# Kernel tuning notes

Measured on AMD Instinct MI355X. Metric: run time of the kernel, lower is better.

Reference implementation:

```python
import jax, jax.numpy as jnp
import numpy as np

D_MODEL = 1024
NUM_HEADS = 16
D_K = D_MODEL // NUM_HEADS
B, S = 4, 2048


def setup_inputs() -> dict:
    key = jax.random.key(0)
    ks = jax.random.split(key, 12)
    scale = 1.0 / np.sqrt(D_MODEL)
    inp = {
        "query": jax.random.normal(ks[0], (B, S, D_MODEL), jnp.float32),
        "key": jax.random.normal(ks[1], (B, S, D_MODEL), jnp.float32),
        "value": jax.random.normal(ks[2], (B, S, D_MODEL), jnp.float32),
        # causal mask, broadcastable over (batch, heads)
        "mask": jnp.tril(jnp.ones((S, S), jnp.int32))[None, None, :, :],
        "Wq": jax.random.normal(ks[3], (D_MODEL, D_MODEL), jnp.float32) * scale,
        "bq": jnp.zeros((D_MODEL,), jnp.float32),
        "Wk": jax.random.normal(ks[4], (D_MODEL, D_MODEL), jnp.float32) * scale,
        "bk": jnp.zeros((D_MODEL,), jnp.float32),
        "Wv": jax.random.normal(ks[5], (D_MODEL, D_MODEL), jnp.float32) * scale,
        "bv": jnp.zeros((D_MODEL,), jnp.float32),
        "Wo": jax.random.normal(ks[6], (D_MODEL, D_MODEL), jnp.float32) * scale,
        "bo": jnp.zeros((D_MODEL,), jnp.float32),
    }
    return inp


def reference(query, key, value, mask, Wq, bq, Wk, bk, Wv, bv, Wo, bo):
    b = query.shape[0]
    # projections (torch Linear: x @ W.T + b)
    Q = query @ Wq.T + bq
    K = key @ Wk.T + bk
    V = value @ Wv.T + bv
    # [B, S, D] -> [B, H, S, d_k]
    def split_heads(x):
        return x.reshape(b, -1, NUM_HEADS, D_K).transpose(0, 2, 1, 3)
    Q, K, V = split_heads(Q), split_heads(K), split_heads(V)
    # scaled dot-product attention, full score matrix as in original
    scores = jnp.einsum("bhqd,bhkd->bhqk", Q, K) / jnp.sqrt(jnp.float32(D_K))
    scores = jnp.where(mask == 0, jnp.float32(-jnp.inf), scores)
    attn = jax.nn.softmax(scores, axis=-1)  # dropout p=0.0 -> identity
    x = jnp.einsum("bhqk,bhkd->bhqd", attn, V)
    # [B, H, S, d_k] -> [B, S, D]
    x = x.transpose(0, 2, 1, 3).reshape(b, -1, D_MODEL)
    return x @ Wo.T + bo
```

## Files before the change

### kernel.cpp

```cpp
#include <hip/hip_runtime.h>
#include <hip/hip_bf16.h>
#include <stdint.h>

#define D_MODEL 1024
#define NUM_HEADS 16
#define DK 64
#define BATCH 4
#define SEQ 2048
#define MTOT (BATCH * SEQ)

typedef unsigned short u16;
typedef unsigned int u32;
typedef __bf16 bf16x8 __attribute__((ext_vector_type(8)));
typedef float f32x4 __attribute__((ext_vector_type(4)));
typedef short s16x4 __attribute__((ext_vector_type(4)));
typedef int   i32x4 __attribute__((ext_vector_type(4)));
typedef int   i32x2 __attribute__((ext_vector_type(2)));
typedef uint  u32x2 __attribute__((ext_vector_type(2)));

__device__ __forceinline__ f32x4 mfma16(s16x4 a, s16x4 b, f32x4 c) {
  return __builtin_amdgcn_mfma_f32_16x16x16bf16_1k(a, b, c, 0, 0, 0);
}

__device__ __forceinline__ u16 f2bf(float f) {
  union { float f; unsigned u; } c; c.f = f;
  unsigned u = c.u + 0x7fffu + ((c.u >> 16) & 1u);
  return (u16)(u >> 16);
}
__device__ __forceinline__ u32 pack_bf2(float f0, float f1) {
  return __builtin_amdgcn_perm(__float_as_uint(f1), __float_as_uint(f0), 0x07060302u);
}
__device__ __forceinline__ s16x4 cast_s16x4(u32 lo, u32 hi) {
  u32x2 t = {lo, hi};
  return (s16x4)t;
}

__device__ __forceinline__ void async16(void* g, void* lds) {
  __builtin_amdgcn_global_load_lds(
      (__attribute__((address_space(1))) void*)g,
      (__attribute__((address_space(3))) void*)lds,
      16, 0, 0);
}
__device__ __forceinline__ void vm_drain() {
  asm volatile("s_waitcnt vmcnt(0)" ::: "memory");
}

struct CvtArgs {
  const float* s[7];
  u16* d[7];
  int n[7];
};
__global__ __launch_bounds__(256)
void cvt_multi(CvtArgs a) {
  const int which = blockIdx.y;
  const int n = a.n[which];
  const int i = (blockIdx.x * 256 + threadIdx.x) * 8;
  if (i >= n) return;
  const float* s = a.s[which];
  u16* d = a.d[which];
  const float4 x = *(const float4*)(s + i);
  const float4 y = *(const float4*)(s + i + 4);
  *(ushort4*)(d + i)     = make_ushort4(f2bf(x.x), f2bf(x.y), f2bf(x.z), f2bf(x.w));
  *(ushort4*)(d + i + 4) = make_ushort4(f2bf(y.x), f2bf(y.y), f2bf(y.z), f2bf(y.w));
}

struct GBatch {
  const u16* A[3]; const u16* W[3]; const float* bias[3];
  void* C[3]; float osc[3]; int mode[3];
};
__global__ __launch_bounds__(256, 2)
void gemm_bt_bias(GBatch ga)
{
  __shared__ __align__(16) u16 smem[16896];
  u16* As0 = smem;
  u16* Bs0 = smem + 4096;
  u16* As1 = smem + 8192;
  u16* Bs1 = smem + 12288;

  const int z = blockIdx.z;
  const u16* __restrict__ A = ga.A[z];
  const u16* __restrict__ W = ga.W[z];
  const float* __restrict__ bias = ga.bias[z];
  void* __restrict__ Cv = ga.C[z];
  const float oscale = ga.osc[z];
  const int mode = ga.mode[z];

  const int t = threadIdx.x;
  const int w = t >> 6, l = t & 63;
  const int quad = l >> 4, lane16 = l & 15;
  const int m0 = blockIdx.x * 128;
  const int n0 = blockIdx.y * 128;
  const int wm = (w >> 1) * 64, wn = (w & 1) * 64;

  const int srow = t >> 2;
  const int scol = (t & 3) * 8;
  const u16* Ag = A + (long)(m0 + srow) * D_MODEL + scol;
  const u16* Wg = W + (long)(n0 + srow) * D_MODEL + scol;

  f32x4 acc[4][4] = {};

  auto stage = [&](u16* As_, u16* Bs_, int k0) {
    async16((void*)(Ag + k0), As_ + w * 512);
    async16((void*)(Ag + 64 * D_MODEL + k0), As_ + w * 512 + 2048);
    async16((void*)(Wg + k0), Bs_ + w * 512);
    async16((void*)(Wg + 64 * D_MODEL + k0), Bs_ + w * 512 + 2048);
  };
  auto compute = [&](const u16* As_, const u16* Bs_) {
    bf16x8 af[4], bfr[4];
#pragma unroll
    for (int i = 0; i < 4; ++i)
      af[i] = *(const bf16x8*)&As_[(wm + i * 16 + lane16) * 32 + quad * 8];
#pragma unroll
    for (int i = 0; i < 4; ++i)
      bfr[i] = *(const bf16x8*)&Bs_[(wn + i * 16 + lane16) * 32 + quad * 8];
#pragma unroll
    for (int i = 0; i < 4; ++i)
#pragma unroll
      for (int jn = 0; jn < 4; ++jn)
        acc[i][jn] = __builtin_amdgcn_mfma_f32_16x16x32_bf16(af[i], bfr[jn], acc[i][jn], 0, 0, 0);
  };

  stage(As0, Bs0, 0);
  vm_drain();
  __syncthreads();
#pragma unroll 1
  for (int k0 = 0; k0 < D_MODEL; k0 += 64) {
    stage(As1, Bs1, k0 + 32);
    compute(As0, Bs0);
    vm_drain();
    __syncthreads();
    if (k0 + 64 < D_MODEL) stage(As0, Bs0, k0 + 64);
    compute(As1, Bs1);
    vm_drain();
    __syncthreads();
  }

  if (mode == 1) {
    u16* T = smem;
#pragma unroll
    for (int jn = 0; jn < 4; ++jn) {
      const int col = wn + jn * 16 + lane16;
      const float bb = bias[n0 + col];
#pragma unroll
      for (int i = 0; i < 4; ++i) {
        const int rbase = wm + i * 16 + quad * 4;
#pragma unroll
        for (int r = 0; r < 4; ++r)
          T[col * 132 + rbase + r] = f2bf((acc[i][jn][r] + bb) * oscale);
      }
    }
    __syncthreads();
    const int bq = m0 >> 11, sbase = m0 & 2047;
    const int a = t & 31;
    const int keystart = ((a >> 3) * 32) + (((a & 7) >> 1) * 4) + ((a & 1) * 16);
    u16* orow = (u16*)Cv + ((long)bq * 1024 + n0) * SEQ + sbase + 4 * a;
#pragma unroll
    for (int pass = 0; pass < 16; ++pass) {
      const int dkl = (t >> 5) + 8 * pass;
      *(u32x2*)(orow + (long)dkl * SEQ) = *(const u32x2*)&T[dkl * 132 + keystart];
    }
  } else {
#pragma unroll
    for (int jn = 0; jn < 4; ++jn) {
      const int col = n0 + wn + jn * 16 + lane16;
      const float bb = bias[col];
#pragma unroll
      for (int i = 0; i < 4; ++i) {
        const int rbase = m0 + wm + i * 16 + quad * 4;
#pragma unroll
        for (int r = 0; r < 4; ++r) {
          const float v = (acc[i][jn][r] + bb) * oscale;
          if (mode == 2) ((float*)Cv)[(long)(rbase + r) * D_MODEL + col] = v;
          else           ((u16*)Cv)[(long)(rbase + r) * D_MODEL + col] = f2bf(v);
        }
      }
    }
  }
}

__global__ __launch_bounds__(256, 3)
void attn_causal(const u16* __restrict__ Q, const u16* __restrict__ K,
                 const u16* __restrict__ VtX, u16* __restrict__ O)
{
  __shared__ __align__(16) u16 Kb[2][32][64];
  __shared__ __align__(16) u16 Vb[2][64][32];
  const int t = threadIdx.x;
  const int w = t >> 6, l = t & 63;
  const int quad = l >> 4, lane16 = l & 15;

  const int lin = blockIdx.x;
  const int xcd = lin & 7;
  const int j = lin >> 3;
  const int bh = xcd * 8 + (j & 7);
  const int g = 15 - (j >> 3);
  const int b = bh >> 4, h = bh & 15;
  const int sw = 4 * g + w;
  const int cmax = 4 * g + 3;
  const int qbase = sw * 32;

  const long qkbase = (long)b * SEQ * D_MODEL + h * DK;

  bf16x8 qf[2][2];
#pragma unroll
  for (int qi = 0; qi < 2; ++qi)
#pragma unroll
    for (int ks = 0; ks < 2; ++ks)
      qf[qi][ks] = *(const bf16x8*)&Q[qkbase +
          (long)(qbase + qi * 16 + lane16) * D_MODEL + ks * 32 + quad * 8];

  const int krow = t >> 3, kc = t & 7;
  const char* Kgt = (const char*)(K + qkbase) + (long)krow * (D_MODEL * 2) + kc * 16;
  u16* KbD0 = &Kb[0][krow][(kc ^ (krow & 7)) * 8];
  u16* KbD1 = &Kb[1][krow][(kc ^ (krow & 7)) * 8];
  const int vrow = t >> 2, vc = t & 3;
  const char* Vgt = (const char*)(VtX + ((long)b * 1024 + h * 64) * SEQ) +
                    (long)vrow * (SEQ * 2) + vc * 16;
  u16* VbD0 = &Vb[0][vrow][(vc ^ (vrow & 3)) * 8];
  u16* VbD1 = &Vb[1][vrow][(vc ^ (vrow & 3)) * 8];

  f32x4 oacc[4][2] = {};
  float lsum[2] = {0.f, 0.f};

  auto body = [&](const u16 (*Kbuf)[64], const u16 (*Vbuf)[32], bool diag) {
    bf16x8 kf[2][2];
#pragma unroll
    for (int kt = 0; kt < 2; ++kt)
#pragma unroll
      for (int ks = 0; ks < 2; ++ks)
        kf[kt][ks] = *(const bf16x8*)
            &Kbuf[kt * 16 + lane16][(((ks * 4 + quad) ^ (lane16 & 7)) * 8)];
    i32x4 vfd[4];
#pragma unroll
    for (int d = 0; d < 4; ++d)
      vfd[d] = *(const i32x4*)
          &Vbuf[d * 16 + lane16][((quad ^ (lane16 & 3)) * 8)];

    f32x4 st[2][2] = {};
    __builtin_amdgcn_s_setprio(1);
#pragma unroll
    for (int kt = 0; kt < 2; ++kt)
#pragma unroll
      for (int qi = 0; qi < 2; ++qi)
#pragma unroll
        for (int ks = 0; ks < 2; ++ks)
          st[kt][qi] = __builtin_amdgcn_mfma_f32_16x16x32_bf16(kf[kt][ks], qf[qi][ks], st[kt][qi], 0, 0, 0);
    __builtin_amdgcn_s_setprio(0);

    u32 pb[2][2][2];
#pragma unroll
    for (int kt = 0; kt < 2; ++kt)
#pragma unroll
      for (int qi = 0; qi < 2; ++qi) {
        float pv[4];
#pragma unroll
        for (int r = 0; r < 4; ++r) {
          float p = __builtin_amdgcn_exp2f(st[kt][qi][r]);
          if (diag && (kt * 16 + quad * 4 + r > qi * 16 + lane16)) p = 0.f;
          pv[r] = p;
        }
        lsum[qi] += (pv[0] + pv[1]) + (pv[2] + pv[3]);
        pb[kt][qi][0] = pack_bf2(pv[0], pv[1]);
        pb[kt][qi][1] = pack_bf2(pv[2], pv[3]);
      }

    __builtin_amdgcn_s_setprio(1);
#pragma unroll
    for (int d = 0; d < 4; ++d) {
      const s16x4 va0 = cast_s16x4((u32)vfd[d].x, (u32)vfd[d].y);
      const s16x4 va1 = cast_s16x4((u32)vfd[d].z, (u32)vfd[d].w);
#pragma unroll
      for (int qi = 0; qi < 2; ++qi) {
        const s16x4 pb0 = cast_s16x4(pb[0][qi][0], pb[0][qi][1]);
        const s16x4 pb1 = cast_s16x4(pb[1][qi][0], pb[1][qi][1]);
        oacc[d][qi] = mfma16(va0, pb0, oacc[d][qi]);
        oacc[d][qi] = mfma16(va1, pb1, oacc[d][qi]);
      }
    }
    __builtin_amdgcn_s_setprio(0);
  };

  {
    i32x4 a0 = *(const i32x4*)(Kgt);
    i32x4 a1 = *(const i32x4*)(Vgt);
    *(i32x4*)KbD0 = a0;
    *(i32x4*)VbD0 = a1;
  }
  i32x4 gKA = *(const i32x4*)(Kgt + 65536);
  i32x4 gVA = *(const i32x4*)(Vgt + 64);
  i32x4 gKB = *(const i32x4*)(Kgt + 2 * 65536);
  i32x4 gVB = *(const i32x4*)(Vgt + 2 * 64);
  __syncthreads();

  for (int c = 0; c <= cmax; c += 2) {
    *(i32x4*)KbD1 = gKA;
    *(i32x4*)VbD1 = gVA;
    if (c + 3 <= cmax) {
      gKA = *(const i32x4*)(Kgt + (long)(c + 3) * 65536);
      gVA = *(const i32x4*)(Vgt + (long)(c + 3) * 64);
    }
    if (c <= sw) body(Kb[0], Vb[0], c == sw);
    __syncthreads();
    if (c + 2 <= cmax) {
      *(i32x4*)KbD0 = gKB;
      *(i32x4*)VbD0 = gVB;
      if (c + 4 <= cmax) {
        gKB = *(const i32x4*)(Kgt + (long)(c + 4) * 65536);
        gVB = *(const i32x4*)(Vgt + (long)(c + 4) * 64);
      }
    }
    if (c + 1 <= sw) body(Kb[1], Vb[1], (c + 1) == sw);
    __syncthreads();
  }

  float linv[2];
#pragma unroll
  for (int qi = 0; qi < 2; ++qi) {
    float v = lsum[qi];
    v += __shfl_xor(v, 16);
    v += __shfl_xor(v, 32);
    linv[qi] = 1.f / v;
  }

#pragma unroll
  for (int qi = 0; qi < 2; ++qi) {
    const long row = (long)b * SEQ + qbase + qi * 16 + lane16;
#pragma unroll
    for (int d = 0; d < 4; ++d) {
      const u32 p0 = ((u32)f2bf(oacc[d][qi][0] * linv[qi])) |
                     ((u32)f2bf(oacc[d][qi][1] * linv[qi]) << 16);
      const u32 p1 = ((u32)f2bf(oacc[d][qi][2] * linv[qi])) |
                     ((u32)f2bf(oacc[d][qi][3] * linv[qi]) << 16);
      u32x2 pk = {p0, p1};
      *(u32x2*)&O[row * D_MODEL + h * 64 + d * 16 + quad * 4] = pk;
    }
  }
}

extern "C" void kernel_launch(void* const* d_in, const int* in_sizes, int n_in,
                              void* d_out, int out_size, void* d_ws, size_t ws_size,
                              hipStream_t stream) {
  const float* q  = (const float*)d_in[0];
  const float* k  = (const float*)d_in[1];
  const float* v  = (const float*)d_in[2];
  const float* Wq = (const float*)d_in[4];
  const float* bq = (const float*)d_in[5];
  const float* Wk = (const float*)d_in[6];
  const float* bk = (const float*)d_in[7];
  const float* Wv = (const float*)d_in[8];
  const float* bv = (const float*)d_in[9];
  const float* Wo = (const float*)d_in[10];
  const float* bo = (const float*)d_in[11];
  float* out = (float*)d_out;

  const size_t NT = (size_t)MTOT * D_MODEL;
  const size_t NW = (size_t)D_MODEL * D_MODEL;

  u16* w0  = (u16*)d_ws;
  u16* qb  = w0;
  u16* kb  = w0 + NT;
  u16* vb  = w0 + 2 * NT;
  u16* Wqb = w0 + 3 * NT;
  u16* Wkb = Wqb + NW;
  u16* Wvb = Wqb + 2 * NW;
  u16* Wob = Wqb + 3 * NW;
  u16* Qp  = (u16*)d_out;
  u16* Kp  = (u16*)d_out + NT;
  u16* Vpt = qb;
  u16* Xp  = kb;

  const dim3 blk(256);

  CvtArgs ca;
  ca.s[0] = q;  ca.d[0] = qb;  ca.n[0] = (int)NT;
  ca.s[1] = k;  ca.d[1] = kb;  ca.n[1] = (int)NT;
  ca.s[2] = v;  ca.d[2] = vb;  ca.n[2] = (int)NT;
  ca.s[3] = Wq; ca.d[3] = Wqb; ca.n[3] = (int)NW;
  ca.s[4] = Wk; ca.d[4] = Wkb; ca.n[4] = (int)NW;
  ca.s[5] = Wv; ca.d[5] = Wvb; ca.n[5] = (int)NW;
  ca.s[6] = Wo; ca.d[6] = Wob; ca.n[6] = (int)NW;
  cvt_multi<<<dim3(4096, 7), blk, 0, stream>>>(ca);

  const float SC = 0.125f * 1.4426950408889634f;

  GBatch g1;
  g1.A[0] = qb; g1.W[0] = Wqb; g1.bias[0] = bq; g1.C[0] = Qp;  g1.osc[0] = SC;  g1.mode[0] = 0;
  g1.A[1] = kb; g1.W[1] = Wkb; g1.bias[1] = bk; g1.C[1] = Kp;  g1.osc[1] = 1.f; g1.mode[1] = 0;
  g1.A[2] = vb; g1.W[2] = Wvb; g1.bias[2] = bv; g1.C[2] = Vpt; g1.osc[2] = 1.f; g1.mode[2] = 1;
  gemm_bt_bias<<<dim3(MTOT / 128, D_MODEL / 128, 3), blk, 0, stream>>>(g1);

  const dim3 agrid(1024);
  attn_causal<<<agrid, blk, 0, stream>>>(Qp, Kp, Vpt, Xp);

  GBatch g2;
  for (int i = 0; i < 3; ++i) {
    g2.A[i] = Xp; g2.W[i] = Wob; g2.bias[i] = bo; g2.C[i] = out;
    g2.osc[i] = 1.f; g2.mode[i] = 2;
  }
  gemm_bt_bias<<<dim3(MTOT / 128, D_MODEL / 128, 1), blk, 0, stream>>>(g2);
}
```

Measured before the change: 316.1 us.

## Triple-buffer GEMM LDS tiles with partial vmcnt waits for deeper prefetch

Replaces the double-buffered K loop in the projection GEMM with a three-stage LDS ring. Loads run two chunks ahead, and each step waits only until the oldest chunk has arrived (vmcnt(4)) rather than draining every outstanding load. This is meant to hide more global-load latency behind the MFMA work. It grows shared memory from about 33KB to 48KB per block, which may limit how many blocks fit on a CU at the launch-bounds target of two.

```diff
diff --git a/kernel.cpp b/kernel.cpp
--- a/kernel.cpp
+++ b/kernel.cpp
@@ -40,9 +40,6 @@
       (__attribute__((address_space(1))) void*)g,
       (__attribute__((address_space(3))) void*)lds,
       16, 0, 0);
-}
-__device__ __forceinline__ void vm_drain() {
-  asm volatile("s_waitcnt vmcnt(0)" ::: "memory");
 }
 
 struct CvtArgs {
@@ -71,12 +68,7 @@
 __global__ __launch_bounds__(256, 2)
 void gemm_bt_bias(GBatch ga)
 {
-  __shared__ __align__(16) u16 smem[16896];
-  u16* As0 = smem;
-  u16* Bs0 = smem + 4096;
-  u16* As1 = smem + 8192;
-  u16* Bs1 = smem + 12288;
-
+  __shared__ __align__(16) u16 smem[24576];
   const int z = blockIdx.z;
   const u16* __restrict__ A = ga.A[z];
   const u16* __restrict__ W = ga.W[z];
@@ -99,13 +91,17 @@
 
   f32x4 acc[4][4] = {};
 
-  auto stage = [&](u16* As_, u16* Bs_, int k0) {
+  auto stage = [&](int buf, int k0) {
+    u16* As_ = smem + buf * 8192;
+    u16* Bs_ = As_ + 4096;
     async16((void*)(Ag + k0), As_ + w * 512);
     async16((void*)(Ag + 64 * D_MODEL + k0), As_ + w * 512 + 2048);
     async16((void*)(Wg + k0), Bs_ + w * 512);
     async16((void*)(Wg + 64 * D_MODEL + k0), Bs_ + w * 512 + 2048);
   };
-  auto compute = [&](const u16* As_, const u16* Bs_) {
+  auto compute = [&](int buf) {
+    const u16* As_ = smem + buf * 8192;
+    const u16* Bs_ = As_ + 4096;
     bf16x8 af[4], bfr[4];
 #pragma unroll
     for (int i = 0; i < 4; ++i)
@@ -120,20 +116,29 @@
         acc[i][jn] = __builtin_amdgcn_mfma_f32_16x16x32_bf16(af[i], bfr[jn], acc[i][jn], 0, 0, 0);
   };
 
-  stage(As0, Bs0, 0);
-  vm_drain();
+  stage(0, 0);
+  stage(1, 32);
+  asm volatile("s_waitcnt vmcnt(4)" ::: "memory");
+  __builtin_amdgcn_s_barrier();
+  __builtin_amdgcn_sched_barrier(0);
+
+  int buf = 0;
+#pragma unroll 1
+  for (int c = 0; c < 32; ++c) {
+    if (c + 2 < 32) stage((buf + 2 >= 3) ? buf - 1 : buf + 2, (c + 2) * 32);
+    compute(buf);
+    if (c < 30) {
+      asm volatile("s_waitcnt vmcnt(4)" ::: "memory");
+      __builtin_amdgcn_s_barrier();
+      __builtin_amdgcn_sched_barrier(0);
+    } else if (c == 30) {
+      asm volatile("s_waitcnt vmcnt(0)" ::: "memory");
+      __builtin_amdgcn_s_barrier();
+      __builtin_amdgcn_sched_barrier(0);
+    }
+    buf = (buf + 1 == 3) ? 0 : buf + 1;
+  }
   __syncthreads();
-#pragma unroll 1
-  for (int k0 = 0; k0 < D_MODEL; k0 += 64) {
-    stage(As1, Bs1, k0 + 32);
-    compute(As0, Bs0);
-    vm_drain();
-    __syncthreads();
-    if (k0 + 64 < D_MODEL) stage(As0, Bs0, k0 + 64);
-    compute(As1, Bs1);
-    vm_drain();
-    __syncthreads();
-  }
 
   if (mode == 1) {
     u16* T = smem;
```

After: 312.3 us. Within noise of the previous version (-1.2%).
